# Performance work log

Measured on AMD Instinct MI355X. Metric: run time of the kernel, lower is better.

Reference implementation:

```python
import math
import jax, jax.numpy as jnp
import numpy as np

N, L, C, H, R = 4, 1024, 1024, 16, 8
HD = C // H
LORA_SCALE = 16.0 / 8.0          # alpha / rank
LOGIT_SCALE_MAX = math.log(100.0)
EPS = 1e-12                      # F.normalize eps


def setup_inputs() -> dict:
    key = jax.random.key(0)
    ks = jax.random.split(key, 10)
    return {
        "x": jax.random.normal(ks[0], (N, L, C), jnp.float32),
        "in_proj_weight": jax.random.normal(ks[1], (3 * C, C), jnp.float32) * 0.02,
        "in_proj_bias": jnp.zeros((3 * C,), jnp.float32),
        "lora_A_q": jax.random.normal(ks[2], (R, C), jnp.float32) * 0.02,
        "lora_B_q": jax.random.normal(ks[3], (C, R), jnp.float32) * 0.02,
        "lora_A_k": jax.random.normal(ks[4], (R, C), jnp.float32) * 0.02,
        "lora_B_k": jax.random.normal(ks[5], (C, R), jnp.float32) * 0.02,
        "lora_A_v": jax.random.normal(ks[6], (R, C), jnp.float32) * 0.02,
        "lora_B_v": jax.random.normal(ks[7], (C, R), jnp.float32) * 0.02,
        "logit_scale": jnp.full((H, 1, 1), math.log(10.0), jnp.float32),
        "out_proj_weight": jax.random.normal(ks[8], (C, C), jnp.float32) * 0.02,
        "out_proj_bias": jnp.zeros((C,), jnp.float32),
    }


def _l2norm(t):
    # matches F.normalize(dim=-1): x / max(||x||, eps)
    n = jnp.sqrt(jnp.sum(t * t, axis=-1, keepdims=True))
    return t / jnp.maximum(n, EPS)


def reference(x, in_proj_weight, in_proj_bias,
              lora_A_q, lora_B_q, lora_A_k, lora_B_k, lora_A_v, lora_B_v,
              logit_scale, out_proj_weight, out_proj_bias):
    # fused QKV projection (frozen base weights)
    qkv = jnp.einsum('nlc,oc->nlo', x, in_proj_weight) + in_proj_bias  # [N,L,3C]
    q0, k0, v0 = jnp.split(qkv, 3, axis=-1)

    # low-rank LoRA adapters: (x A^T) B^T * scale
    def lora(A, B):
        return jnp.einsum('nlr,cr->nlc', jnp.einsum('nlc,rc->nlr', x, A), B) * LORA_SCALE

    q = q0 + lora(lora_A_q, lora_B_q)
    k = k0 + lora(lora_A_k, lora_B_k)
    v = v0 + lora(lora_A_v, lora_B_v)

    # [N,L,C] -> [N,H,L,HD]
    def heads(t):
        return t.reshape(N, L, H, HD).transpose(0, 2, 1, 3)

    q, k, v = heads(q), heads(k), heads(v)

    # cosine-similarity attention with clamped learnable per-head logit scale
    attn = jnp.einsum('nhld,nhmd->nhlm', _l2norm(q), _l2norm(k))
    scale = jnp.exp(jnp.minimum(logit_scale, LOGIT_SCALE_MAX))  # [H,1,1]
    attn = jax.nn.softmax(attn * scale, axis=-1)

    out = jnp.einsum('nhlm,nhmd->nhld', attn, v)  # [N,H,L,HD]
    out = out.transpose(0, 2, 1, 3).reshape(N, L, C)

    return jnp.einsum('nlc,oc->nlo', out, out_proj_weight) + out_proj_bias
```

## Files before the change

kernel.cpp:

```cpp
#include <hip/hip_runtime.h>
#include <hip/hip_bf16.h>
#include <cstdint>
#include <cstddef>

#define DEVI __device__ __forceinline__

typedef __attribute__((ext_vector_type(8))) short bf16x8;
typedef __attribute__((ext_vector_type(4))) float f32x4;
typedef __attribute__((ext_vector_type(8))) unsigned short u16x8;

DEVI unsigned short f2bf(float f) {
  union { float f; unsigned int u; } v; v.f = f;
  unsigned int r = v.u + 0x7FFFu + ((v.u >> 16) & 1u);
  return (unsigned short)(r >> 16);
}

DEVI void gload_lds16(const void* g, void* l) {
  __builtin_amdgcn_global_load_lds((const __attribute__((address_space(1))) void*)g,
                                   (__attribute__((address_space(3))) void*)l,
                                   16, 0, 0);
}

__global__ void cvt_k(const float* __restrict__ in, unsigned short* __restrict__ out, int n4) {
  int i = blockIdx.x * 256 + threadIdx.x;
  if (i >= n4) return;
  float4 v = reinterpret_cast<const float4*>(in)[i];
  ushort4 o;
  o.x = f2bf(v.x); o.y = f2bf(v.y); o.z = f2bf(v.z); o.w = f2bf(v.w);
  reinterpret_cast<ushort4*>(out)[i] = o;
}

__global__ void weff_k(const float* __restrict__ W,
                       const float* __restrict__ Aq, const float* __restrict__ Bq,
                       const float* __restrict__ Ak, const float* __restrict__ Bk,
                       const float* __restrict__ Av, const float* __restrict__ Bv,
                       unsigned short* __restrict__ out) {
  int idx = blockIdx.x * 256 + threadIdx.x;
  int o = idx >> 10, c = idx & 1023;
  const float* A; const float* B; int ol;
  if (o < 1024)      { A = Aq; B = Bq; ol = o; }
  else if (o < 2048) { A = Ak; B = Bk; ol = o - 1024; }
  else               { A = Av; B = Bv; ol = o - 2048; }
  float acc = W[idx];
#pragma unroll
  for (int r = 0; r < 8; ++r) acc += 2.0f * B[ol*8 + r] * A[r*1024 + c];
  out[idx] = f2bf(acc);
}

template<int NCOLS, int EPI>
__global__ __launch_bounds__(256)
void gemm_k(const unsigned short* __restrict__ A,
            const unsigned short* __restrict__ Bw,
            const float* __restrict__ bias,
            unsigned short* __restrict__ q_out,
            unsigned short* __restrict__ k_out,
            unsigned short* __restrict__ v_out,
            float* __restrict__ f_out)
{
  constexpr int K = 1024;
  constexpr int NBN = NCOLS / 128;
  __shared__ unsigned short As[128*32];
  __shared__ unsigned short Bs[128*32];
  const int bid  = blockIdx.x;
  const int bn   = bid % NBN, bm = bid / NBN;
  const int tid  = threadIdx.x;
  const int lane = tid & 63, wave = tid >> 6;
  const int wr = wave >> 1, wc = wave & 1;
  const int l15 = lane & 15, g = lane >> 4;

  const f32x4 fzero = {0.f, 0.f, 0.f, 0.f};
  f32x4 acc[4][4];
#pragma unroll
  for (int m = 0; m < 4; ++m)
#pragma unroll
    for (int n = 0; n < 4; ++n) acc[m][n] = fzero;

  for (int k0 = 0; k0 < K; k0 += 32) {
#pragma unroll
    for (int j = 0; j < 2; ++j) {
      int off = j*4096 + tid*16;
      int r = off >> 6, cb = off & 63;
      gload_lds16((const char*)(A  + (size_t)(bm*128 + r) * K) + k0*2 + cb, (char*)As + off);
      gload_lds16((const char*)(Bw + (size_t)(bn*128 + r) * K) + k0*2 + cb, (char*)Bs + off);
    }
    __syncthreads();
    bf16x8 af[4], bfr[4];
#pragma unroll
    for (int m = 0; m < 4; ++m)
      af[m] = *(const bf16x8*)((const char*)As + (wr*64 + m*16 + l15)*64 + g*16);
#pragma unroll
    for (int n = 0; n < 4; ++n)
      bfr[n] = *(const bf16x8*)((const char*)Bs + (wc*64 + n*16 + l15)*64 + g*16);
#pragma unroll
    for (int m = 0; m < 4; ++m)
#pragma unroll
      for (int n = 0; n < 4; ++n)
        acc[m][n] = __builtin_amdgcn_mfma_f32_16x16x32_bf16(af[m], bfr[n], acc[m][n], 0, 0, 0);
    __syncthreads();
  }

  const int colBase = bn*128 + wc*64;
  const int rBase   = bm*128 + wr*64;
  float bias_n[4];
#pragma unroll
  for (int n = 0; n < 4; ++n) bias_n[n] = bias[colBase + n*16 + l15];
#pragma unroll
  for (int m = 0; m < 4; ++m)
#pragma unroll
    for (int n = 0; n < 4; ++n)
#pragma unroll
      for (int r = 0; r < 4; ++r) acc[m][n][r] += bias_n[n];

  if constexpr (EPI == 0) {
    const int sec = colBase >> 10;
    const int h = (colBase & 1023) >> 6;
    if (sec < 2) {
#pragma unroll
      for (int m = 0; m < 4; ++m)
#pragma unroll
        for (int r = 0; r < 4; ++r) {
          float ss = 0.f;
#pragma unroll
          for (int n = 0; n < 4; ++n) { float x = acc[m][n][r]; ss += x*x; }
          ss += __shfl_xor(ss, 1);
          ss += __shfl_xor(ss, 2);
          ss += __shfl_xor(ss, 4);
          ss += __shfl_xor(ss, 8);
          float inv = 1.0f / fmaxf(sqrtf(ss), 1e-12f);
#pragma unroll
          for (int n = 0; n < 4; ++n) acc[m][n][r] *= inv;
        }
      unsigned short* dst = (sec == 0) ? q_out : k_out;
#pragma unroll
      for (int m = 0; m < 4; ++m)
#pragma unroll
        for (int r = 0; r < 4; ++r) {
          int mrow = rBase + m*16 + g*4 + r;
          int nidx = mrow >> 10, li = mrow & 1023;
          size_t base = (((size_t)(nidx*16 + h))*1024 + li)*64;
#pragma unroll
          for (int n = 0; n < 4; ++n)
            dst[base + n*16 + l15] = f2bf(acc[m][n][r]);
        }
    } else {
      unsigned short* pool = (wave & 1) ? Bs : As;
      const int nidx = rBase >> 10;
      const size_t gbase = ((size_t)(nidx*16 + h) * 64) * 1024 + (rBase & 1023);
#pragma unroll
      for (int round = 0; round < 2; ++round) {
        if ((wave >> 1) == round) {
#pragma unroll
          for (int m = 0; m < 4; ++m)
#pragma unroll
            for (int n = 0; n < 4; ++n) {
              ushort4 pk;
              pk.x = f2bf(acc[m][n][0]); pk.y = f2bf(acc[m][n][1]);
              pk.z = f2bf(acc[m][n][2]); pk.w = f2bf(acc[m][n][3]);
              int d_loc = n*16 + l15;
              int li    = m*16 + g*4;
              *(ushort4*)((char*)pool + d_loc*128 + ((li*2) ^ ((d_loc & 7) << 4))) = pk;
            }
#pragma unroll
          for (int p = 0; p < 8; ++p) {
            int d_loc = p*8 + (lane >> 3);
            int lic   = (lane & 7) * 8;
            u16x8 row = *(const u16x8*)((const char*)pool + d_loc*128 + ((lic*2) ^ ((d_loc & 7) << 4)));
            *(u16x8*)(v_out + gbase + (size_t)d_loc*1024 + lic) = row;
          }
        }
        __syncthreads();
      }
    }
  } else {
#pragma unroll
    for (int m = 0; m < 4; ++m)
#pragma unroll
      for (int r = 0; r < 4; ++r) {
        int mrow = rBase + m*16 + g*4 + r;
#pragma unroll
        for (int n = 0; n < 4; ++n)
          f_out[(size_t)mrow*NCOLS + colBase + n*16 + l15] = acc[m][n][r];
      }
  }
}

__global__ __launch_bounds__(256)
void attn_k(const unsigned short* __restrict__ qh,
            const unsigned short* __restrict__ kh,
            const unsigned short* __restrict__ vt,
            const float* __restrict__ logit_scale,
            unsigned short* __restrict__ ao)
{
  __shared__ unsigned short Ks [2][4096];
  __shared__ unsigned short VTs[2][4096];
  __shared__ unsigned short Ps [4][1024];
  const int bid = blockIdx.x;
  const int xcd = bid & 7, slot = bid >> 3;
  const int nh = xcd + ((slot >> 4) << 3);
  const int qb = slot & 15;
  const int h = nh & 15;
  const int tid = threadIdx.x;
  const int w = tid >> 6, lane = tid & 63;
  const int l15 = lane & 15, g = lane >> 4;
  const float s = __expf(fminf(logit_scale[h], 4.6051701859880914f));

  const unsigned short* Qb  = qh + ((size_t)nh*1024 + qb*64) * 64;
  const unsigned short* Kb  = kh + (size_t)nh * 1024 * 64;
  const unsigned short* Vtb = vt + (size_t)nh * 64 * 1024;

  bf16x8 qf[2];
#pragma unroll
  for (int kk = 0; kk < 2; ++kk)
    qf[kk] = *(const bf16x8*)(Qb + (w*16 + l15)*64 + kk*32 + g*8);

  const f32x4 fzero = {0.f, 0.f, 0.f, 0.f};
  f32x4 oacc[4];
#pragma unroll
  for (int n = 0; n < 4; ++n) oacc[n] = fzero;
  float rs[4] = {0.f, 0.f, 0.f, 0.f};

#define STAGE(b, kt)                                                              \
  {                                                                               \
    _Pragma("unroll")                                                             \
    for (int j = 0; j < 2; ++j) {                                                 \
      int off = j*4096 + tid*16;                                                  \
      int r = off >> 7, cb = off & 127;                                           \
      int scb = cb ^ ((r & 7) << 4);                                              \
      gload_lds16((const char*)Kb  + (size_t)((kt)*64 + r)*128 + scb,             \
                  (char*)Ks[b] + off);                                            \
      gload_lds16((const char*)Vtb + (size_t)r*2048 + (kt)*128 + scb,             \
                  (char*)VTs[b] + off);                                           \
    }                                                                             \
  }

  STAGE(0, 0);
  __syncthreads();

  for (int kt = 0; kt < 16; ++kt) {
    const int cur = kt & 1;
    if (kt < 15) STAGE(cur ^ 1, kt + 1);

    f32x4 sf[4];
#pragma unroll
    for (int n = 0; n < 4; ++n) sf[n] = fzero;
#pragma unroll
    for (int n = 0; n < 4; ++n) {
      int krow = n*16 + l15;
      int sw = (krow & 7) << 4;
#pragma unroll
      for (int kk = 0; kk < 2; ++kk) {
        bf16x8 bfr = *(const bf16x8*)((const char*)Ks[cur] + krow*128 + ((kk*64 + g*16) ^ sw));
        sf[n] = __builtin_amdgcn_mfma_f32_16x16x32_bf16(qf[kk], bfr, sf[n], 0, 0, 0);
      }
    }

#pragma unroll
    for (int n = 0; n < 4; ++n)
#pragma unroll
      for (int r = 0; r < 4; ++r) {
        float p = __expf(s * sf[n][r]);
        rs[r] += p;
        int prow = g*4 + r;
        int swp = ((prow >> 2) & 3) << 5;
        *(unsigned short*)((char*)Ps[w] + prow*128 + (((n*16 + l15)*2) ^ swp)) = f2bf(p);
      }

#pragma unroll
    for (int kk = 0; kk < 2; ++kk) {
      int swp = ((l15 >> 2) & 3) << 5;
      bf16x8 af = *(const bf16x8*)((const char*)Ps[w] + l15*128 + ((kk*64 + g*16) ^ swp));
#pragma unroll
      for (int n = 0; n < 4; ++n) {
        int vrow = n*16 + l15;
        bf16x8 bfv = *(const bf16x8*)((const char*)VTs[cur] + vrow*128 + ((kk*64 + g*16) ^ ((vrow & 7) << 4)));
        oacc[n] = __builtin_amdgcn_mfma_f32_16x16x32_bf16(af, bfv, oacc[n], 0, 0, 0);
      }
    }
    __syncthreads();
  }
#undef STAGE

#pragma unroll
  for (int r = 0; r < 4; ++r) {
    rs[r] += __shfl_xor(rs[r], 1);
    rs[r] += __shfl_xor(rs[r], 2);
    rs[r] += __shfl_xor(rs[r], 4);
    rs[r] += __shfl_xor(rs[r], 8);
  }
  const int nidx = nh >> 4;
#pragma unroll
  for (int r = 0; r < 4; ++r) {
    float inv = 1.0f / rs[r];
    int qrow = qb*64 + w*16 + g*4 + r;
    size_t rowoff = (size_t)(nidx*1024 + qrow) * 1024 + h*64;
#pragma unroll
    for (int n = 0; n < 4; ++n)
      ao[rowoff + n*16 + l15] = f2bf(oacc[n][r] * inv);
  }
}

extern "C" void kernel_launch(void* const* d_in, const int* in_sizes, int n_in,
                              void* d_out, int out_size, void* d_ws, size_t ws_size,
                              hipStream_t stream) {
  const float* x    = (const float*)d_in[0];
  const float* Wqkv = (const float*)d_in[1];
  const float* bqkv = (const float*)d_in[2];
  const float* Aq   = (const float*)d_in[3];
  const float* Bq   = (const float*)d_in[4];
  const float* Ak   = (const float*)d_in[5];
  const float* Bk   = (const float*)d_in[6];
  const float* Av   = (const float*)d_in[7];
  const float* Bv   = (const float*)d_in[8];
  const float* ls   = (const float*)d_in[9];
  const float* Wout = (const float*)d_in[10];
  const float* bout = (const float*)d_in[11];
  float* out = (float*)d_out;

  char* ws = (char*)d_ws;
  unsigned short* xb   = (unsigned short*)(ws);
  unsigned short* weff = (unsigned short*)(ws + (8u  << 20));
  unsigned short* wob  = (unsigned short*)(ws + (14u << 20));
  unsigned short* qhp  = (unsigned short*)(ws + (16u << 20));
  unsigned short* khp  = (unsigned short*)(ws + (24u << 20));
  unsigned short* vtp  = (unsigned short*)(ws + (32u << 20));
  unsigned short* aop  = xb;

  cvt_k <<<4096, 256, 0, stream>>>(x, xb, 1048576);
  cvt_k <<<1024, 256, 0, stream>>>(Wout, wob, 262144);
  weff_k<<<12288, 256, 0, stream>>>(Wqkv, Aq, Bq, Ak, Bk, Av, Bv, weff);

  gemm_k<3072, 0><<<768, 256, 0, stream>>>(xb, weff, bqkv, qhp, khp, vtp, nullptr);
  attn_k<<<1024, 256, 0, stream>>>(qhp, khp, vtp, ls, aop);
  gemm_k<1024, 1><<<256, 256, 0, stream>>>(aop, wob, bout, nullptr, nullptr, nullptr, out);
}
```

Before: 215.0 us.

## Process two query tiles per attention block and parallelize V transpose epilogue

```diff
diff --git a/kernel.cpp b/kernel.cpp
--- a/kernel.cpp
+++ b/kernel.cpp
@@ -143,32 +143,27 @@
             dst[base + n*16 + l15] = f2bf(acc[m][n][r]);
         }
     } else {
-      unsigned short* pool = (wave & 1) ? Bs : As;
+      __shared__ unsigned short Vp[2][4096];
+      unsigned short* pool = (wave == 0) ? As : (wave == 1) ? Bs : &Vp[wave - 2][0];
       const int nidx = rBase >> 10;
       const size_t gbase = ((size_t)(nidx*16 + h) * 64) * 1024 + (rBase & 1023);
 #pragma unroll
-      for (int round = 0; round < 2; ++round) {
-        if ((wave >> 1) == round) {
-#pragma unroll
-          for (int m = 0; m < 4; ++m)
-#pragma unroll
-            for (int n = 0; n < 4; ++n) {
-              ushort4 pk;
-              pk.x = f2bf(acc[m][n][0]); pk.y = f2bf(acc[m][n][1]);
-              pk.z = f2bf(acc[m][n][2]); pk.w = f2bf(acc[m][n][3]);
-              int d_loc = n*16 + l15;
-              int li    = m*16 + g*4;
-              *(ushort4*)((char*)pool + d_loc*128 + ((li*2) ^ ((d_loc & 7) << 4))) = pk;
-            }
-#pragma unroll
-          for (int p = 0; p < 8; ++p) {
-            int d_loc = p*8 + (lane >> 3);
-            int lic   = (lane & 7) * 8;
-            u16x8 row = *(const u16x8*)((const char*)pool + d_loc*128 + ((lic*2) ^ ((d_loc & 7) << 4)));
-            *(u16x8*)(v_out + gbase + (size_t)d_loc*1024 + lic) = row;
-          }
-        }
-        __syncthreads();
+      for (int m = 0; m < 4; ++m)
+#pragma unroll
+        for (int n = 0; n < 4; ++n) {
+          ushort4 pk;
+          pk.x = f2bf(acc[m][n][0]); pk.y = f2bf(acc[m][n][1]);
+          pk.z = f2bf(acc[m][n][2]); pk.w = f2bf(acc[m][n][3]);
+          int d_loc = n*16 + l15;
+          int li    = m*16 + g*4;
+          *(ushort4*)((char*)pool + d_loc*128 + ((li*2) ^ ((d_loc & 7) << 4))) = pk;
+        }
+#pragma unroll
+      for (int p = 0; p < 8; ++p) {
+        int d_loc = p*8 + (lane >> 3);
+        int lic   = (lane & 7) * 8;
+        u16x8 row = *(const u16x8*)((const char*)pool + d_loc*128 + ((lic*2) ^ ((d_loc & 7) << 4)));
+        *(u16x8*)(v_out + gbase + (size_t)d_loc*1024 + lic) = row;
       }
     }
   } else {
@@ -196,28 +191,32 @@
   __shared__ unsigned short Ps [4][1024];
   const int bid = blockIdx.x;
   const int xcd = bid & 7, slot = bid >> 3;
-  const int nh = xcd + ((slot >> 4) << 3);
-  const int qb = slot & 15;
+  const int nh = xcd + ((slot >> 3) << 3);
+  const int qp = slot & 7;
   const int h = nh & 15;
   const int tid = threadIdx.x;
   const int w = tid >> 6, lane = tid & 63;
   const int l15 = lane & 15, g = lane >> 4;
   const float s = __expf(fminf(logit_scale[h], 4.6051701859880914f));
 
-  const unsigned short* Qb  = qh + ((size_t)nh*1024 + qb*64) * 64;
+  const unsigned short* Qb  = qh + (size_t)nh * 1024 * 64;
   const unsigned short* Kb  = kh + (size_t)nh * 1024 * 64;
   const unsigned short* Vtb = vt + (size_t)nh * 64 * 1024;
 
-  bf16x8 qf[2];
-#pragma unroll
-  for (int kk = 0; kk < 2; ++kk)
-    qf[kk] = *(const bf16x8*)(Qb + (w*16 + l15)*64 + kk*32 + g*8);
+  bf16x8 qf[2][2];
+#pragma unroll
+  for (int u = 0; u < 2; ++u)
+#pragma unroll
+    for (int kk = 0; kk < 2; ++kk)
+      qf[u][kk] = *(const bf16x8*)(Qb + (size_t)(qp*128 + u*64 + w*16 + l15)*64 + kk*32 + g*8);
 
   const f32x4 fzero = {0.f, 0.f, 0.f, 0.f};
-  f32x4 oacc[4];
-#pragma unroll
-  for (int n = 0; n < 4; ++n) oacc[n] = fzero;
-  float rs[4] = {0.f, 0.f, 0.f, 0.f};
+  f32x4 oacc[2][4];
+#pragma unroll
+  for (int u = 0; u < 2; ++u)
+#pragma unroll
+    for (int n = 0; n < 4; ++n) oacc[u][n] = fzero;
+  float rs[2][4] = {{0.f,0.f,0.f,0.f},{0.f,0.f,0.f,0.f}};
 
 #define STAGE(b, kt)                                                              \
   {                                                                               \
@@ -240,40 +239,43 @@
     const int cur = kt & 1;
     if (kt < 15) STAGE(cur ^ 1, kt + 1);
 
-    f32x4 sf[4];
-#pragma unroll
-    for (int n = 0; n < 4; ++n) sf[n] = fzero;
-#pragma unroll
-    for (int n = 0; n < 4; ++n) {
-      int krow = n*16 + l15;
-      int sw = (krow & 7) << 4;
+#pragma unroll
+    for (int u = 0; u < 2; ++u) {
+      f32x4 sf[4];
+#pragma unroll
+      for (int n = 0; n < 4; ++n) sf[n] = fzero;
+#pragma unroll
+      for (int n = 0; n < 4; ++n) {
+        int krow = n*16 + l15;
+        int sw = (krow & 7) << 4;
+#pragma unroll
+        for (int kk = 0; kk < 2; ++kk) {
+          bf16x8 bfr = *(const bf16x8*)((const char*)Ks[cur] + krow*128 + ((kk*64 + g*16) ^ sw));
+          sf[n] = __builtin_amdgcn_mfma_f32_16x16x32_bf16(qf[u][kk], bfr, sf[n], 0, 0, 0);
+        }
+      }
+
+#pragma unroll
+      for (int n = 0; n < 4; ++n)
+#pragma unroll
+        for (int r = 0; r < 4; ++r) {
+          float p = __expf(s * sf[n][r]);
+          rs[u][r] += p;
+          int prow = g*4 + r;
+          int swp = ((prow >> 2) & 3) << 5;
+          *(unsigned short*)((char*)Ps[w] + prow*128 + (((n*16 + l15)*2) ^ swp)) = f2bf(p);
+        }
+
 #pragma unroll
       for (int kk = 0; kk < 2; ++kk) {
-        bf16x8 bfr = *(const bf16x8*)((const char*)Ks[cur] + krow*128 + ((kk*64 + g*16) ^ sw));
-        sf[n] = __builtin_amdgcn_mfma_f32_16x16x32_bf16(qf[kk], bfr, sf[n], 0, 0, 0);
-      }
-    }
-
-#pragma unroll
-    for (int n = 0; n < 4; ++n)
-#pragma unroll
-      for (int r = 0; r < 4; ++r) {
-        float p = __expf(s * sf[n][r]);
-        rs[r] += p;
-        int prow = g*4 + r;
-        int swp = ((prow >> 2) & 3) << 5;
-        *(unsigned short*)((char*)Ps[w] + prow*128 + (((n*16 + l15)*2) ^ swp)) = f2bf(p);
-      }
-
-#pragma unroll
-    for (int kk = 0; kk < 2; ++kk) {
-      int swp = ((l15 >> 2) & 3) << 5;
-      bf16x8 af = *(const bf16x8*)((const char*)Ps[w] + l15*128 + ((kk*64 + g*16) ^ swp));
-#pragma unroll
-      for (int n = 0; n < 4; ++n) {
-        int vrow = n*16 + l15;
-        bf16x8 bfv = *(const bf16x8*)((const char*)VTs[cur] + vrow*128 + ((kk*64 + g*16) ^ ((vrow & 7) << 4)));
-        oacc[n] = __builtin_amdgcn_mfma_f32_16x16x32_bf16(af, bfv, oacc[n], 0, 0, 0);
+        int swp = ((l15 >> 2) & 3) << 5;
+        bf16x8 af = *(const bf16x8*)((const char*)Ps[w] + l15*128 + ((kk*64 + g*16) ^ swp));
+#pragma unroll
+        for (int n = 0; n < 4; ++n) {
+          int vrow = n*16 + l15;
+          bf16x8 bfv = *(const bf16x8*)((const char*)VTs[cur] + vrow*128 + ((kk*64 + g*16) ^ ((vrow & 7) << 4)));
+          oacc[u][n] = __builtin_amdgcn_mfma_f32_16x16x32_bf16(af, bfv, oacc[u][n], 0, 0, 0);
+        }
       }
     }
     __syncthreads();
@@ -281,22 +283,26 @@
 #undef STAGE
 
 #pragma unroll
-  for (int r = 0; r < 4; ++r) {
-    rs[r] += __shfl_xor(rs[r], 1);
-    rs[r] += __shfl_xor(rs[r], 2);
-    rs[r] += __shfl_xor(rs[r], 4);
-    rs[r] += __shfl_xor(rs[r], 8);
-  }
+  for (int u = 0; u < 2; ++u)
+#pragma unroll
+    for (int r = 0; r < 4; ++r) {
+      rs[u][r] += __shfl_xor(rs[u][r], 1);
+      rs[u][r] += __shfl_xor(rs[u][r], 2);
+      rs[u][r] += __shfl_xor(rs[u][r], 4);
+      rs[u][r] += __shfl_xor(rs[u][r], 8);
+    }
   const int nidx = nh >> 4;
 #pragma unroll
-  for (int r = 0; r < 4; ++r) {
-    float inv = 1.0f / rs[r];
-    int qrow = qb*64 + w*16 + g*4 + r;
-    size_t rowoff = (size_t)(nidx*1024 + qrow) * 1024 + h*64;
-#pragma unroll
-    for (int n = 0; n < 4; ++n)
-      ao[rowoff + n*16 + l15] = f2bf(oacc[n][r] * inv);
-  }
+  for (int u = 0; u < 2; ++u)
+#pragma unroll
+    for (int r = 0; r < 4; ++r) {
+      float inv = 1.0f / rs[u][r];
+      int qrow = qp*128 + u*64 + w*16 + g*4 + r;
+      size_t rowoff = (size_t)(nidx*1024 + qrow) * 1024 + h*64;
+#pragma unroll
+      for (int n = 0; n < 4; ++n)
+        ao[rowoff + n*16 + l15] = f2bf(oacc[u][n][r] * inv);
+    }
 }
 
 extern "C" void kernel_launch(void* const* d_in, const int* in_sizes, int n_in,
@@ -330,6 +336,6 @@
   weff_k<<<12288, 256, 0, stream>>>(Wqkv, Aq, Bq, Ak, Bk, Av, Bv, weff);
 
   gemm_k<3072, 0><<<768, 256, 0, stream>>>(xb, weff, bqkv, qhp, khp, vtp, nullptr);
-  attn_k<<<1024, 256, 0, stream>>>(qhp, khp, vtp, ls, aop);
+  attn_k<<<512, 256, 0, stream>>>(qhp, khp, vtp, ls, aop);
   gemm_k<1024, 1><<<256, 256, 0, stream>>>(aop, wob, bout, nullptr, nullptr, nullptr, out);
 }
```

New measurement: 203.5 us. 5.4% less time.
